# Kernel tuning notes

Measured on AMD Instinct MI355X. Metric: run time of the kernel, lower is better.

The kernel has to match this reference:

```python
import jax, jax.numpy as jnp
import numpy as np

MAX_SPAN = 8
NEG_INF = -1e9


def _enumerate_spans(seq_len, max_span):
    starts, ends = [], []
    for i in range(seq_len):
        for j in range(i, min(i + max_span, seq_len)):
            starts.append(i)
            ends.append(j)
    return np.asarray(starts, np.int32), np.asarray(ends, np.int32)


def setup_inputs() -> dict:
    key = jax.random.key(0)
    ks = jax.random.split(key, 12)
    B, S, Hd = 8, 256, 768
    R, Wd = 256, 32
    raw_dim = 3 * Hd + Wd
    s = lambda d: 1.0 / np.sqrt(d)
    return {
        "H": jax.random.normal(ks[0], (B, S, Hd), jnp.float32),
        "attention_mask": jnp.ones((B, S), jnp.float32),
        "W_width": jax.random.normal(ks[1], (MAX_SPAN + 1, Wd), jnp.float32) * 0.02,
        "w_attn": jax.random.normal(ks[2], (Hd,), jnp.float32) * s(Hd),
        "b_attn": jnp.zeros((), jnp.float32),
        "W_span": jax.random.normal(ks[3], (raw_dim, R), jnp.float32) * s(raw_dim),
        "b_span": jnp.zeros((R,), jnp.float32),
        "w_asp": jax.random.normal(ks[4], (R,), jnp.float32) * s(R),
        "b_asp": jnp.zeros((), jnp.float32),
        "w_opn": jax.random.normal(ks[5], (R,), jnp.float32) * s(R),
        "b_opn": jnp.zeros((), jnp.float32),
        "W_nasp": jax.random.normal(ks[6], (Hd, R), jnp.float32) * s(Hd),
        "b_nasp": jnp.zeros((R,), jnp.float32),
        "W_nopn": jax.random.normal(ks[7], (Hd, R), jnp.float32) * s(Hd),
        "b_nopn": jnp.zeros((R,), jnp.float32),
    }


def reference(H, attention_mask, W_width, w_attn, b_attn, W_span, b_span,
              w_asp, b_asp, w_opn, b_opn, W_nasp, b_nasp, W_nopn, b_nopn):
    B, S, Hd = H.shape
    starts, ends = _enumerate_spans(S, MAX_SPAN)  # static numpy, (N,)
    widths = ends - starts + 1                    # (N,)
    offs = starts[:, None] + np.arange(MAX_SPAN)[None, :]  # (N, L)
    valid = jnp.asarray(offs <= ends[:, None])             # (N, L) bool
    idx = jnp.asarray(np.clip(offs, 0, S - 1))              # (N, L)

    # attention logits per token, computed once (fused form of per-span attn_proj)
    logits = H @ w_attn + b_attn                  # (B, S)
    win_logits = logits[:, idx]                   # (B, N, L)
    win_logits = jnp.where(valid[None], win_logits, NEG_INF)
    attn = jax.nn.softmax(win_logits, axis=-1)    # (B, N, L)
    tokens = H[:, idx, :]                         # (B, N, L, Hd)
    pooled = jnp.einsum('bnl,bnlh->bnh', attn, tokens)

    h_starts = H[:, jnp.asarray(starts), :]       # (B, N, Hd)
    h_ends = H[:, jnp.asarray(ends), :]
    e_width = W_width[jnp.asarray(widths)]        # (N, Wd)
    e_width = jnp.broadcast_to(e_width[None], (B,) + e_width.shape)

    raw = jnp.concatenate([h_starts, h_ends, pooled, e_width], axis=-1)
    span_reprs = jax.nn.relu(raw @ W_span + b_span)  # dropout inactive (eval)

    asp_scores = span_reprs @ w_asp + b_asp       # (B, N)
    opn_scores = span_reprs @ w_opn + b_opn

    lengths = jnp.clip(attention_mask.sum(axis=1, keepdims=True), 1.0)
    h_mean = (H * attention_mask[..., None]).sum(axis=1) / lengths
    null_asp = jnp.tanh(h_mean @ W_nasp + b_nasp)
    null_opn = jnp.tanh(h_mean @ W_nopn + b_nopn)

    return span_reprs, asp_scores, opn_scores, null_asp, null_opn
```

## Files before the change

kernel.cpp:

```cpp
#include <hip/hip_runtime.h>
#include <math.h>

#define S 256
#define HD 768
#define RR 256
#define NSPAN 2020
#define BB 8

typedef __attribute__((ext_vector_type(8))) short bf16x8;
typedef __attribute__((ext_vector_type(4))) float f32x4;

__device__ inline ushort f2bf(float x) {
    union { float f; unsigned u; } v; v.f = x;
    unsigned r = v.u + 0x7FFF + ((v.u >> 16) & 1);
    return (ushort)(r >> 16);
}

__global__ __launch_bounds__(256) void k_pre(const float* __restrict__ H,
                                             const float* __restrict__ w_attn,
                                             const float* __restrict__ b_attn,
                                             const float* __restrict__ mask,
                                             const float* __restrict__ Wspan,
                                             const float* __restrict__ W_width,
                                             ushort* __restrict__ Hb,
                                             float* __restrict__ logits,
                                             ushort* __restrict__ Wt,
                                             float* __restrict__ hmean,
                                             float* __restrict__ EW) {
    __shared__ __align__(16) char smem[16640];
    int bid = blockIdx.x;
    int tid = threadIdx.x;

    if (bid < 96) {
        float (*red)[64] = (float(*)[64])smem;
        float* msum = (float*)(smem + 1024);
        int b = bid & 7, hb = bid >> 3;
        int sg = tid >> 6, hl = tid & 63;
        int h = hb * 64 + hl;
        const float* Hbase = H + (size_t)b * S * HD + h;
        const float* mbase = mask + b * S;
        float a0 = 0.f, a1 = 0.f, a2 = 0.f, a3 = 0.f;
        #pragma unroll
        for (int s2 = 0; s2 < S; s2 += 16) {
            int s = s2 + sg;
            a0 += Hbase[(size_t)(s)      * HD] * mbase[s];
            a1 += Hbase[(size_t)(s + 4)  * HD] * mbase[s + 4];
            a2 += Hbase[(size_t)(s + 8)  * HD] * mbase[s + 8];
            a3 += Hbase[(size_t)(s + 12) * HD] * mbase[s + 12];
        }
        float acc = (a0 + a1) + (a2 + a3);
        float mv = mbase[tid];
        for (int off = 32; off; off >>= 1) mv += __shfl_down(mv, off);
        if (hl == 0) msum[sg] = mv;
        red[sg][hl] = acc;
        __syncthreads();
        if (sg == 0) {
            float ms = msum[0] + msum[1] + msum[2] + msum[3];
            float len = ms < 1.f ? 1.f : ms;
            hmean[b * HD + h] = (red[0][hl] + red[1][hl] + red[2][hl] + red[3][hl]) / len;
        }
    } else if (bid < 240) {
        float (*tile)[65] = (float(*)[65])smem;
        int idx = bid - 96;
        int hb = idx % 12, rb = (idx / 12) & 3, c = idx / 48;
        for (int e = tid; e < 4096; e += 256) {
            int hl = e >> 6, rl = e & 63;
            tile[hl][rl] = Wspan[(size_t)(c * 768 + hb * 64 + hl) * 256 + rb * 64 + rl];
        }
        __syncthreads();
        for (int e = tid; e < 4096; e += 256) {
            int rl = e >> 6, hl = e & 63;
            Wt[(size_t)(c * 256 + rb * 64 + rl) * 768 + hb * 64 + hl] = f2bf(tile[hl][rl]);
        }
    } else if (bid < 752) {
        int pb = bid - 240;
        int wv = tid >> 6, lane = tid & 63;
        int row = pb * 4 + wv;
        const float4* h4 = (const float4*)(H + (size_t)row * HD);
        const float4* w4 = (const float4*)w_attn;
        float acc = 0.f;
        #pragma unroll
        for (int k = 0; k < 3; ++k) {
            float4 a = h4[k * 64 + lane];
            float4 w = w4[k * 64 + lane];
            acc += a.x * w.x + a.y * w.y + a.z * w.z + a.w * w.w;
            ushort4 o;
            o.x = f2bf(a.x); o.y = f2bf(a.y); o.z = f2bf(a.z); o.w = f2bf(a.w);
            *(ushort4*)(Hb + (size_t)row * HD + k * 256 + lane * 4) = o;
        }
        for (int off = 32; off; off >>= 1) acc += __shfl_down(acc, off);
        if (lane == 0) logits[row] = acc + b_attn[0];
    } else {
        int w = bid - 752;
        int r = tid;
        float acc = 0.f;
        for (int k = 0; k < 32; ++k)
            acc += W_width[w * 32 + k] * Wspan[(size_t)(2304 + k) * RR + r];
        EW[w * RR + r] = acc;
    }
}

__global__ __launch_bounds__(256) void k_mid(const ushort* __restrict__ Hb,
                                             const ushort* __restrict__ Wt,
                                             float* __restrict__ P,
                                             const float* __restrict__ hmean,
                                             const float* __restrict__ W_nasp,
                                             const float* __restrict__ b_nasp,
                                             const float* __restrict__ W_nopn,
                                             const float* __restrict__ b_nopn,
                                             float* __restrict__ out_nasp,
                                             float* __restrict__ out_nopn) {
    __shared__ __align__(16) char smem[32768];
    int bid = blockIdx.x;
    int tid = threadIdx.x;

    if (bid < 384) {
        char* lds = smem;
        int mt = bid & 31, nt = bid >> 5;
        int m0 = mt * 64, n0 = nt * 64;
        int wv = tid >> 6, lane = tid & 63;
        int wm = (wv >> 1) * 32, wn = (wv & 1) * 32;

        int ck8 = ((lane & 7) ^ (lane >> 3)) * 8;
        int issue0 = wv * 2;
        int srowA = issue0 * 8 + (lane >> 3);
        int srowB = srowA + 8;

        auto STAGE = [&](int buf, int k0) {
            char* dst = lds + buf * 16384;
            __builtin_amdgcn_global_load_lds(
                (const __attribute__((address_space(1))) void*)(Hb + (size_t)(m0 + srowA) * HD + k0 + ck8),
                (__attribute__((address_space(3))) void*)(dst + issue0 * 1024), 16, 0, 0);
            __builtin_amdgcn_global_load_lds(
                (const __attribute__((address_space(1))) void*)(Wt + (size_t)(n0 + srowA) * HD + k0 + ck8),
                (__attribute__((address_space(3))) void*)(dst + 8192 + issue0 * 1024), 16, 0, 0);
            __builtin_amdgcn_global_load_lds(
                (const __attribute__((address_space(1))) void*)(Hb + (size_t)(m0 + srowB) * HD + k0 + ck8),
                (__attribute__((address_space(3))) void*)(dst + issue0 * 1024 + 1024), 16, 0, 0);
            __builtin_amdgcn_global_load_lds(
                (const __attribute__((address_space(1))) void*)(Wt + (size_t)(n0 + srowB) * HD + k0 + ck8),
                (__attribute__((address_space(3))) void*)(dst + 8192 + issue0 * 1024 + 1024), 16, 0, 0);
        };

        f32x4 acc[2][2] = {};

        STAGE(0, 0);
        __syncthreads();
        int cur = 0;
        #pragma unroll 1
        for (int t = 0; t < 12; ++t) {
            if (t + 1 < 12) STAGE(cur ^ 1, (t + 1) * 64);
            char* cb = lds + cur * 16384;
            #pragma unroll
            for (int ks = 0; ks < 2; ++ks) {
                int kb = ks * 64 + ((lane >> 4) * 16);
                bf16x8 af[2], bfr[2];
                #pragma unroll
                for (int f = 0; f < 2; ++f) {
                    int ar = wm + f * 16 + (lane & 15);
                    af[f] = *(const bf16x8*)(cb + ar * 128 + (kb ^ ((ar & 7) << 4)));
                    int br = wn + f * 16 + (lane & 15);
                    bfr[f] = *(const bf16x8*)(cb + 8192 + br * 128 + (kb ^ ((br & 7) << 4)));
                }
                #pragma unroll
                for (int f = 0; f < 2; ++f)
                    #pragma unroll
                    for (int j = 0; j < 2; ++j)
                        acc[f][j] = __builtin_amdgcn_mfma_f32_16x16x32_bf16(af[f], bfr[j], acc[f][j], 0, 0, 0);
            }
            __syncthreads();
            cur ^= 1;
        }

        #pragma unroll
        for (int f = 0; f < 2; ++f) {
            #pragma unroll
            for (int j = 0; j < 2; ++j) {
                int col = n0 + wn + j * 16 + (lane & 15);
                size_t pb = (size_t)(col >> 8) * 524288 + (col & 255);
                #pragma unroll
                for (int rg = 0; rg < 4; ++rg) {
                    int row = m0 + wm + f * 16 + (lane >> 4) * 4 + rg;
                    P[pb + (size_t)row * 256] = acc[f][j][rg];
                }
            }
        }
    } else {
        float* hm = (float*)smem;
        float (*ra)[32] = (float(*)[32])(smem + 4096);
        float (*ro)[32] = (float(*)[32])(smem + 5120);
        int idx = bid - 384;
        int b = idx >> 3, rc = idx & 7;
        int c = tid & 31, hc = tid >> 5;
        int r = rc * 32 + c;
        for (int h = tid; h < HD; h += 256) hm[h] = hmean[b * HD + h];
        __syncthreads();
        float a = 0.f, o = 0.f;
        for (int h = hc * 96; h < hc * 96 + 96; ++h) {
            float x = hm[h];
            a += x * W_nasp[(size_t)h * RR + r];
            o += x * W_nopn[(size_t)h * RR + r];
        }
        ra[hc][c] = a; ro[hc][c] = o;
        __syncthreads();
        if (tid < 32) {
            float sa = 0.f, so = 0.f;
            #pragma unroll
            for (int u = 0; u < 8; ++u) { sa += ra[u][tid]; so += ro[u][tid]; }
            int rr = rc * 32 + tid;
            out_nasp[b * RR + rr] = tanhf(sa + b_nasp[rr]);
            out_nopn[b * RR + rr] = tanhf(so + b_nopn[rr]);
        }
    }
}

__global__ __launch_bounds__(64) void k_span4(const float* __restrict__ logits,
                                              const float* __restrict__ P,
                                              const float* __restrict__ EW,
                                              const float* __restrict__ b_span,
                                              const float* __restrict__ w_asp,
                                              const float* __restrict__ b_asp,
                                              const float* __restrict__ w_opn,
                                              const float* __restrict__ b_opn,
                                              float* __restrict__ out_repr,
                                              float* __restrict__ out_asp,
                                              float* __restrict__ out_opn) {
    int bid = blockIdx.x;
    int id = (bid & 7) * 256 + (bid >> 3);
    int b = id >> 8;
    int start = id & 255;
    int nw = 256 - start; if (nw > 8) nw = 8;
    int t = threadIdx.x;

    int nbase;
    if (start <= 248) nbase = start * 8;
    else { int tt = start - 249; nbase = 1992 + 7 * tt - (tt * (tt - 1)) / 2; }

    float E[8], inv[8];
    {
        float lg[8];
        float M = -INFINITY;
        #pragma unroll
        for (int l = 0; l < 8; ++l) {
            lg[l] = (l < nw) ? logits[b * S + start + l] : -INFINITY;
            M = fmaxf(M, lg[l]);
        }
        float run = 0.f;
        #pragma unroll
        for (int l = 0; l < 8; ++l) {
            E[l] = (l < nw) ? __expf(lg[l] - M) : 0.f;
            run += E[l];
            inv[l] = 1.f / run;
        }
    }

    size_t rb = ((size_t)b * S + start) * 64 + t;
    const f32x4* P04 = (const f32x4*)P;
    const f32x4* P14 = (const f32x4*)(P + 524288);
    const f32x4* P24 = (const f32x4*)(P + 1048576);

    f32x4 p0 = P04[rb];
    f32x4 bs = ((const f32x4*)b_span)[t];
    f32x4 wa = ((const f32x4*)w_asp)[t];
    f32x4 wo = ((const f32x4*)w_opn)[t];
    f32x4 num = {0.f, 0.f, 0.f, 0.f};
    float pa[8], po[8];

    #pragma unroll
    for (int j = 0; j < 8; ++j) {
        f32x4 p2 = P24[rb + (size_t)j * 64];
        f32x4 p1 = P14[rb + (size_t)j * 64];
        f32x4 ewj = ((const f32x4*)EW)[(j + 1) * 64 + t];
        num += E[j] * p2;
        f32x4 pre = p0 + p1 + num * inv[j] + ewj + bs;
        f32x4 v;
        v[0] = fmaxf(pre[0], 0.f);
        v[1] = fmaxf(pre[1], 0.f);
        v[2] = fmaxf(pre[2], 0.f);
        v[3] = fmaxf(pre[3], 0.f);
        if (j < nw)
            *(f32x4*)(out_repr + ((size_t)b * NSPAN + nbase + j) * RR + t * 4) = v;
        pa[j] = v[0] * wa[0] + v[1] * wa[1] + v[2] * wa[2] + v[3] * wa[3];
        po[j] = v[0] * wo[0] + v[1] * wo[1] + v[2] * wo[2] + v[3] * wo[3];
    }

    #pragma unroll
    for (int j = 0; j < 8; ++j) {
        if (j < nw) {
            float a = pa[j], o = po[j];
            #pragma unroll
            for (int off = 32; off; off >>= 1) {
                a += __shfl_down(a, off);
                o += __shfl_down(o, off);
            }
            if (t == 0) {
                size_t oi = (size_t)b * NSPAN + nbase + j;
                out_asp[oi] = a + b_asp[0];
                out_opn[oi] = o + b_opn[0];
            }
        }
    }
}

extern "C" void kernel_launch(void* const* d_in, const int* in_sizes, int n_in,
                              void* d_out, int out_size, void* d_ws, size_t ws_size,
                              hipStream_t stream) {
    const float* H       = (const float*)d_in[0];
    const float* mask    = (const float*)d_in[1];
    const float* W_width = (const float*)d_in[2];
    const float* w_attn  = (const float*)d_in[3];
    const float* b_attn  = (const float*)d_in[4];
    const float* W_span  = (const float*)d_in[5];
    const float* b_span  = (const float*)d_in[6];
    const float* w_asp   = (const float*)d_in[7];
    const float* b_asp   = (const float*)d_in[8];
    const float* w_opn   = (const float*)d_in[9];
    const float* b_opn   = (const float*)d_in[10];
    const float* W_nasp  = (const float*)d_in[11];
    const float* b_nasp  = (const float*)d_in[12];
    const float* W_nopn  = (const float*)d_in[13];
    const float* b_nopn  = (const float*)d_in[14];

    float* out  = (float*)d_out;
    float* repr = out;
    float* asp  = out + (size_t)BB * NSPAN * RR;
    float* opn  = asp + (size_t)BB * NSPAN;
    float* nasp = opn + (size_t)BB * NSPAN;
    float* nopn = nasp + (size_t)BB * RR;

    float* ws     = (float*)d_ws;
    float* logits = ws;
    float* hmean  = ws + 2048;
    float* EW     = ws + 8192;
    float* P      = ws + 10496;
    ushort* Hb    = (ushort*)(P + 1572864);
    ushort* Wt    = Hb + (size_t)2048 * 768;

    k_pre<<<dim3(761), dim3(256), 0, stream>>>(H, w_attn, b_attn, mask, W_span, W_width,
                                               Hb, logits, Wt, hmean, EW);
    k_mid<<<dim3(448), dim3(256), 0, stream>>>(Hb, Wt, P, hmean,
                                               W_nasp, b_nasp, W_nopn, b_nopn, nasp, nopn);
    k_span4<<<dim3(BB * S), dim3(64), 0, stream>>>(logits, P, EW, b_span, w_asp, b_asp,
                                                   w_opn, b_opn, repr, asp, opn);
}
```

Measured before the change: 29.92 us.

## Redistribute side computations across kernels to shorten the GEMM critical path

```diff
diff --git a/kernel.cpp b/kernel.cpp
--- a/kernel.cpp
+++ b/kernel.cpp
@@ -16,53 +16,16 @@
     return (ushort)(r >> 16);
 }
 
-__global__ __launch_bounds__(256) void k_pre(const float* __restrict__ H,
-                                             const float* __restrict__ w_attn,
-                                             const float* __restrict__ b_attn,
-                                             const float* __restrict__ mask,
+__global__ __launch_bounds__(256) void k_cvt(const float* __restrict__ H,
                                              const float* __restrict__ Wspan,
-                                             const float* __restrict__ W_width,
                                              ushort* __restrict__ Hb,
-                                             float* __restrict__ logits,
-                                             ushort* __restrict__ Wt,
-                                             float* __restrict__ hmean,
-                                             float* __restrict__ EW) {
-    __shared__ __align__(16) char smem[16640];
+                                             ushort* __restrict__ Wt) {
+    __shared__ __align__(16) float tile[64][65];
     int bid = blockIdx.x;
     int tid = threadIdx.x;
 
-    if (bid < 96) {
-        float (*red)[64] = (float(*)[64])smem;
-        float* msum = (float*)(smem + 1024);
-        int b = bid & 7, hb = bid >> 3;
-        int sg = tid >> 6, hl = tid & 63;
-        int h = hb * 64 + hl;
-        const float* Hbase = H + (size_t)b * S * HD + h;
-        const float* mbase = mask + b * S;
-        float a0 = 0.f, a1 = 0.f, a2 = 0.f, a3 = 0.f;
-        #pragma unroll
-        for (int s2 = 0; s2 < S; s2 += 16) {
-            int s = s2 + sg;
-            a0 += Hbase[(size_t)(s)      * HD] * mbase[s];
-            a1 += Hbase[(size_t)(s + 4)  * HD] * mbase[s + 4];
-            a2 += Hbase[(size_t)(s + 8)  * HD] * mbase[s + 8];
-            a3 += Hbase[(size_t)(s + 12) * HD] * mbase[s + 12];
-        }
-        float acc = (a0 + a1) + (a2 + a3);
-        float mv = mbase[tid];
-        for (int off = 32; off; off >>= 1) mv += __shfl_down(mv, off);
-        if (hl == 0) msum[sg] = mv;
-        red[sg][hl] = acc;
-        __syncthreads();
-        if (sg == 0) {
-            float ms = msum[0] + msum[1] + msum[2] + msum[3];
-            float len = ms < 1.f ? 1.f : ms;
-            hmean[b * HD + h] = (red[0][hl] + red[1][hl] + red[2][hl] + red[3][hl]) / len;
-        }
-    } else if (bid < 240) {
-        float (*tile)[65] = (float(*)[65])smem;
-        int idx = bid - 96;
-        int hb = idx % 12, rb = (idx / 12) & 3, c = idx / 48;
+    if (bid < 144) {
+        int hb = bid % 12, rb = (bid / 12) & 3, c = bid / 48;
         for (int e = tid; e < 4096; e += 256) {
             int hl = e >> 6, rl = e & 63;
             tile[hl][rl] = Wspan[(size_t)(c * 768 + hb * 64 + hl) * 256 + rb * 64 + rl];
@@ -72,53 +35,42 @@
             int rl = e >> 6, hl = e & 63;
             Wt[(size_t)(c * 256 + rb * 64 + rl) * 768 + hb * 64 + hl] = f2bf(tile[hl][rl]);
         }
-    } else if (bid < 752) {
-        int pb = bid - 240;
+    } else {
+        int idx = bid - 144;
         int wv = tid >> 6, lane = tid & 63;
-        int row = pb * 4 + wv;
+        int row = idx * 4 + wv;
         const float4* h4 = (const float4*)(H + (size_t)row * HD);
-        const float4* w4 = (const float4*)w_attn;
-        float acc = 0.f;
         #pragma unroll
         for (int k = 0; k < 3; ++k) {
             float4 a = h4[k * 64 + lane];
-            float4 w = w4[k * 64 + lane];
-            acc += a.x * w.x + a.y * w.y + a.z * w.z + a.w * w.w;
             ushort4 o;
             o.x = f2bf(a.x); o.y = f2bf(a.y); o.z = f2bf(a.z); o.w = f2bf(a.w);
             *(ushort4*)(Hb + (size_t)row * HD + k * 256 + lane * 4) = o;
         }
-        for (int off = 32; off; off >>= 1) acc += __shfl_down(acc, off);
-        if (lane == 0) logits[row] = acc + b_attn[0];
-    } else {
-        int w = bid - 752;
-        int r = tid;
-        float acc = 0.f;
-        for (int k = 0; k < 32; ++k)
-            acc += W_width[w * 32 + k] * Wspan[(size_t)(2304 + k) * RR + r];
-        EW[w * RR + r] = acc;
     }
 }
 
-__global__ __launch_bounds__(256) void k_mid(const ushort* __restrict__ Hb,
-                                             const ushort* __restrict__ Wt,
-                                             float* __restrict__ P,
-                                             const float* __restrict__ hmean,
-                                             const float* __restrict__ W_nasp,
-                                             const float* __restrict__ b_nasp,
-                                             const float* __restrict__ W_nopn,
-                                             const float* __restrict__ b_nopn,
-                                             float* __restrict__ out_nasp,
-                                             float* __restrict__ out_nopn) {
+__global__ __launch_bounds__(256) void k_mid2(const ushort* __restrict__ Hb,
+                                              const ushort* __restrict__ Wt,
+                                              const float* __restrict__ H,
+                                              const float* __restrict__ mask,
+                                              const float* __restrict__ w_attn,
+                                              const float* __restrict__ b_attn,
+                                              const float* __restrict__ Wspan,
+                                              const float* __restrict__ W_width,
+                                              float* __restrict__ P,
+                                              float* __restrict__ hmean,
+                                              float* __restrict__ logits,
+                                              float* __restrict__ EW) {
     __shared__ __align__(16) char smem[32768];
     int bid = blockIdx.x;
     int tid = threadIdx.x;
+    int wv = tid >> 6, lane = tid & 63;
 
     if (bid < 384) {
         char* lds = smem;
         int mt = bid & 31, nt = bid >> 5;
         int m0 = mt * 64, n0 = nt * 64;
-        int wv = tid >> 6, lane = tid & 63;
         int wm = (wv >> 1) * 32, wn = (wv & 1) * 32;
 
         int ck8 = ((lane & 7) ^ (lane >> 3)) * 8;
@@ -185,36 +137,60 @@
                 }
             }
         }
+    } else if (bid < 480) {
+        float (*red)[64] = (float(*)[64])smem;
+        float* msum = (float*)(smem + 1024);
+        int idx = bid - 384;
+        int b = idx & 7, hb = idx >> 3;
+        int sg = wv, hl = lane;
+        int h = hb * 64 + hl;
+        const float* Hbase = H + (size_t)b * S * HD + h;
+        const float* mbase = mask + b * S;
+        float a0 = 0.f, a1 = 0.f, a2 = 0.f, a3 = 0.f;
+        #pragma unroll
+        for (int s2 = 0; s2 < S; s2 += 16) {
+            int s = s2 + sg;
+            a0 += Hbase[(size_t)(s)      * HD] * mbase[s];
+            a1 += Hbase[(size_t)(s + 4)  * HD] * mbase[s + 4];
+            a2 += Hbase[(size_t)(s + 8)  * HD] * mbase[s + 8];
+            a3 += Hbase[(size_t)(s + 12) * HD] * mbase[s + 12];
+        }
+        float acc = (a0 + a1) + (a2 + a3);
+        float mv = mbase[tid];
+        for (int off = 32; off; off >>= 1) mv += __shfl_down(mv, off);
+        if (hl == 0) msum[sg] = mv;
+        red[sg][hl] = acc;
+        __syncthreads();
+        if (sg == 0) {
+            float ms = msum[0] + msum[1] + msum[2] + msum[3];
+            float len = ms < 1.f ? 1.f : ms;
+            hmean[b * HD + h] = (red[0][hl] + red[1][hl] + red[2][hl] + red[3][hl]) / len;
+        }
+    } else if (bid < 992) {
+        int idx = bid - 480;
+        int row = idx * 4 + wv;
+        const float4* h4 = (const float4*)(H + (size_t)row * HD);
+        const float4* w4 = (const float4*)w_attn;
+        float acc = 0.f;
+        #pragma unroll
+        for (int k = 0; k < 3; ++k) {
+            float4 a = h4[k * 64 + lane];
+            float4 w = w4[k * 64 + lane];
+            acc += a.x * w.x + a.y * w.y + a.z * w.z + a.w * w.w;
+        }
+        for (int off = 32; off; off >>= 1) acc += __shfl_down(acc, off);
+        if (lane == 0) logits[row] = acc + b_attn[0];
     } else {
-        float* hm = (float*)smem;
-        float (*ra)[32] = (float(*)[32])(smem + 4096);
-        float (*ro)[32] = (float(*)[32])(smem + 5120);
-        int idx = bid - 384;
-        int b = idx >> 3, rc = idx & 7;
-        int c = tid & 31, hc = tid >> 5;
-        int r = rc * 32 + c;
-        for (int h = tid; h < HD; h += 256) hm[h] = hmean[b * HD + h];
-        __syncthreads();
-        float a = 0.f, o = 0.f;
-        for (int h = hc * 96; h < hc * 96 + 96; ++h) {
-            float x = hm[h];
-            a += x * W_nasp[(size_t)h * RR + r];
-            o += x * W_nopn[(size_t)h * RR + r];
-        }
-        ra[hc][c] = a; ro[hc][c] = o;
-        __syncthreads();
-        if (tid < 32) {
-            float sa = 0.f, so = 0.f;
-            #pragma unroll
-            for (int u = 0; u < 8; ++u) { sa += ra[u][tid]; so += ro[u][tid]; }
-            int rr = rc * 32 + tid;
-            out_nasp[b * RR + rr] = tanhf(sa + b_nasp[rr]);
-            out_nopn[b * RR + rr] = tanhf(so + b_nopn[rr]);
-        }
+        int w = bid - 992;
+        int r = tid;
+        float acc = 0.f;
+        for (int k = 0; k < 32; ++k)
+            acc += W_width[w * 32 + k] * Wspan[(size_t)(2304 + k) * RR + r];
+        EW[w * RR + r] = acc;
     }
 }
 
-__global__ __launch_bounds__(64) void k_span4(const float* __restrict__ logits,
+__global__ __launch_bounds__(64) void k_span5(const float* __restrict__ logits,
                                               const float* __restrict__ P,
                                               const float* __restrict__ EW,
                                               const float* __restrict__ b_span,
@@ -222,82 +198,116 @@
                                               const float* __restrict__ b_asp,
                                               const float* __restrict__ w_opn,
                                               const float* __restrict__ b_opn,
+                                              const float* __restrict__ hmean,
+                                              const float* __restrict__ W_nasp,
+                                              const float* __restrict__ b_nasp,
+                                              const float* __restrict__ W_nopn,
+                                              const float* __restrict__ b_nopn,
                                               float* __restrict__ out_repr,
                                               float* __restrict__ out_asp,
-                                              float* __restrict__ out_opn) {
+                                              float* __restrict__ out_opn,
+                                              float* __restrict__ out_nasp,
+                                              float* __restrict__ out_nopn) {
+    __shared__ float hm[HD];
+    __shared__ float ra[2][32], ro[2][32];
     int bid = blockIdx.x;
-    int id = (bid & 7) * 256 + (bid >> 3);
-    int b = id >> 8;
-    int start = id & 255;
-    int nw = 256 - start; if (nw > 8) nw = 8;
     int t = threadIdx.x;
 
-    int nbase;
-    if (start <= 248) nbase = start * 8;
-    else { int tt = start - 249; nbase = 1992 + 7 * tt - (tt * (tt - 1)) / 2; }
-
-    float E[8], inv[8];
-    {
-        float lg[8];
-        float M = -INFINITY;
-        #pragma unroll
-        for (int l = 0; l < 8; ++l) {
-            lg[l] = (l < nw) ? logits[b * S + start + l] : -INFINITY;
-            M = fmaxf(M, lg[l]);
-        }
-        float run = 0.f;
-        #pragma unroll
-        for (int l = 0; l < 8; ++l) {
-            E[l] = (l < nw) ? __expf(lg[l] - M) : 0.f;
-            run += E[l];
-            inv[l] = 1.f / run;
-        }
-    }
-
-    size_t rb = ((size_t)b * S + start) * 64 + t;
-    const f32x4* P04 = (const f32x4*)P;
-    const f32x4* P14 = (const f32x4*)(P + 524288);
-    const f32x4* P24 = (const f32x4*)(P + 1048576);
-
-    f32x4 p0 = P04[rb];
-    f32x4 bs = ((const f32x4*)b_span)[t];
-    f32x4 wa = ((const f32x4*)w_asp)[t];
-    f32x4 wo = ((const f32x4*)w_opn)[t];
-    f32x4 num = {0.f, 0.f, 0.f, 0.f};
-    float pa[8], po[8];
-
-    #pragma unroll
-    for (int j = 0; j < 8; ++j) {
-        f32x4 p2 = P24[rb + (size_t)j * 64];
-        f32x4 p1 = P14[rb + (size_t)j * 64];
-        f32x4 ewj = ((const f32x4*)EW)[(j + 1) * 64 + t];
-        num += E[j] * p2;
-        f32x4 pre = p0 + p1 + num * inv[j] + ewj + bs;
-        f32x4 v;
-        v[0] = fmaxf(pre[0], 0.f);
-        v[1] = fmaxf(pre[1], 0.f);
-        v[2] = fmaxf(pre[2], 0.f);
-        v[3] = fmaxf(pre[3], 0.f);
-        if (j < nw)
-            *(f32x4*)(out_repr + ((size_t)b * NSPAN + nbase + j) * RR + t * 4) = v;
-        pa[j] = v[0] * wa[0] + v[1] * wa[1] + v[2] * wa[2] + v[3] * wa[3];
-        po[j] = v[0] * wo[0] + v[1] * wo[1] + v[2] * wo[2] + v[3] * wo[3];
-    }
-
-    #pragma unroll
-    for (int j = 0; j < 8; ++j) {
-        if (j < nw) {
-            float a = pa[j], o = po[j];
+    if (bid < 2048) {
+        int id = (bid & 7) * 256 + (bid >> 3);
+        int b = id >> 8;
+        int start = id & 255;
+        int nw = 256 - start; if (nw > 8) nw = 8;
+
+        int nbase;
+        if (start <= 248) nbase = start * 8;
+        else { int tt = start - 249; nbase = 1992 + 7 * tt - (tt * (tt - 1)) / 2; }
+
+        float E[8], inv[8];
+        {
+            float lg[8];
+            float M = -INFINITY;
             #pragma unroll
-            for (int off = 32; off; off >>= 1) {
-                a += __shfl_down(a, off);
-                o += __shfl_down(o, off);
-            }
-            if (t == 0) {
-                size_t oi = (size_t)b * NSPAN + nbase + j;
-                out_asp[oi] = a + b_asp[0];
-                out_opn[oi] = o + b_opn[0];
-            }
+            for (int l = 0; l < 8; ++l) {
+                lg[l] = (l < nw) ? logits[b * S + start + l] : -INFINITY;
+                M = fmaxf(M, lg[l]);
+            }
+            float run = 0.f;
+            #pragma unroll
+            for (int l = 0; l < 8; ++l) {
+                E[l] = (l < nw) ? __expf(lg[l] - M) : 0.f;
+                run += E[l];
+                inv[l] = 1.f / run;
+            }
+        }
+
+        size_t rb = ((size_t)b * S + start) * 64 + t;
+        const f32x4* P04 = (const f32x4*)P;
+        const f32x4* P14 = (const f32x4*)(P + 524288);
+        const f32x4* P24 = (const f32x4*)(P + 1048576);
+
+        f32x4 p0 = P04[rb];
+        f32x4 bs = ((const f32x4*)b_span)[t];
+        f32x4 wa = ((const f32x4*)w_asp)[t];
+        f32x4 wo = ((const f32x4*)w_opn)[t];
+        f32x4 num = {0.f, 0.f, 0.f, 0.f};
+        float pa[8], po[8];
+
+        #pragma unroll
+        for (int j = 0; j < 8; ++j) {
+            f32x4 p2 = P24[rb + (size_t)j * 64];
+            f32x4 p1 = P14[rb + (size_t)j * 64];
+            f32x4 ewj = ((const f32x4*)EW)[(j + 1) * 64 + t];
+            num += E[j] * p2;
+            f32x4 pre = p0 + p1 + num * inv[j] + ewj + bs;
+            f32x4 v;
+            v[0] = fmaxf(pre[0], 0.f);
+            v[1] = fmaxf(pre[1], 0.f);
+            v[2] = fmaxf(pre[2], 0.f);
+            v[3] = fmaxf(pre[3], 0.f);
+            if (j < nw)
+                *(f32x4*)(out_repr + ((size_t)b * NSPAN + nbase + j) * RR + t * 4) = v;
+            pa[j] = v[0] * wa[0] + v[1] * wa[1] + v[2] * wa[2] + v[3] * wa[3];
+            po[j] = v[0] * wo[0] + v[1] * wo[1] + v[2] * wo[2] + v[3] * wo[3];
+        }
+
+        #pragma unroll
+        for (int j = 0; j < 8; ++j) {
+            if (j < nw) {
+                float a = pa[j], o = po[j];
+                #pragma unroll
+                for (int off = 32; off; off >>= 1) {
+                    a += __shfl_down(a, off);
+                    o += __shfl_down(o, off);
+                }
+                if (t == 0) {
+                    size_t oi = (size_t)b * NSPAN + nbase + j;
+                    out_asp[oi] = a + b_asp[0];
+                    out_opn[oi] = o + b_opn[0];
+                }
+            }
+        }
+    } else {
+        int idx = bid - 2048;
+        int b = idx >> 3, rc = idx & 7;
+        int c = t & 31, hc = t >> 5;
+        int r = rc * 32 + c;
+        for (int h = t; h < HD; h += 64) hm[h] = hmean[b * HD + h];
+        __syncthreads();
+        float a = 0.f, o = 0.f;
+        for (int h = hc * 384; h < hc * 384 + 384; ++h) {
+            float x = hm[h];
+            a += x * W_nasp[(size_t)h * RR + r];
+            o += x * W_nopn[(size_t)h * RR + r];
+        }
+        ra[hc][c] = a; ro[hc][c] = o;
+        __syncthreads();
+        if (t < 32) {
+            float sa = ra[0][t] + ra[1][t];
+            float so = ro[0][t] + ro[1][t];
+            int rr = rc * 32 + t;
+            out_nasp[b * RR + rr] = tanhf(sa + b_nasp[rr]);
+            out_nopn[b * RR + rr] = tanhf(so + b_nopn[rr]);
         }
     }
 }
@@ -336,10 +346,10 @@
     ushort* Hb    = (ushort*)(P + 1572864);
     ushort* Wt    = Hb + (size_t)2048 * 768;
 
-    k_pre<<<dim3(761), dim3(256), 0, stream>>>(H, w_attn, b_attn, mask, W_span, W_width,
-                                               Hb, logits, Wt, hmean, EW);
-    k_mid<<<dim3(448), dim3(256), 0, stream>>>(Hb, Wt, P, hmean,
-                                               W_nasp, b_nasp, W_nopn, b_nopn, nasp, nopn);
-    k_span4<<<dim3(BB * S), dim3(64), 0, stream>>>(logits, P, EW, b_span, w_asp, b_asp,
-                                                   w_opn, b_opn, repr, asp, opn);
-}
+    k_cvt<<<dim3(656), dim3(256), 0, stream>>>(H, W_span, Hb, Wt);
+    k_mid2<<<dim3(1001), dim3(256), 0, stream>>>(Hb, Wt, H, mask, w_attn, b_attn,
+                                                 W_span, W_width, P, hmean, logits, EW);
+    k_span5<<<dim3(2112), dim3(64), 0, stream>>>(logits, P, EW, b_span, w_asp, b_asp,
+                                                 w_opn, b_opn, hmean, W_nasp, b_nasp,
+                                                 W_nopn, b_nopn, repr, asp, opn, nasp, nopn);
+}
```

Measured after the change: 44.18 us. 1.48x slower.
